# Kernel optimization log

Measured on AMD Instinct MI355X. Metric: run time of the kernel, lower is better.

The kernel has to match this reference:

```python
import jax, jax.numpy as jnp
import numpy as np

N = 50000   # nodes
E = 400000  # edges (before self-loops)
F = 128     # num_features
H = 8       # heads (layer 1)
C = 64      # hidden_channels
B = 64      # graphs in batch
K = 10      # num_classes
NEG_SLOPE = 0.2


def setup_inputs() -> dict:
    key = jax.random.key(0)
    ks = jax.random.split(key, 12)
    g = lambda k, shape, fan: jax.random.normal(k, shape, jnp.float32) / np.sqrt(fan).astype(np.float32)
    return {
        "x": jax.random.normal(ks[0], (N, F), jnp.float32),
        "edge_index": jax.random.randint(ks[1], (2, E), 0, N, jnp.int32),
        "batch": jnp.sort(jax.random.randint(ks[2], (N,), 0, B, jnp.int32)),
        "W1": g(ks[3], (F, H * C), F),
        "att_src1": g(ks[4], (H, C), C),
        "att_dst1": g(ks[5], (H, C), C),
        "b1": jnp.zeros((H * C,), jnp.float32),
        "W2": g(ks[6], (H * C, C), H * C),
        "att_src2": g(ks[7], (1, C), C),
        "att_dst2": g(ks[8], (1, C), C),
        "b2": jnp.zeros((C,), jnp.float32),
        "lin1_w": g(ks[9], (C, C), C),
        "lin1_b": jnp.zeros((C,), jnp.float32),
        "lin2_w": g(ks[10], (C, K), C),
        "lin2_b": jnp.zeros((K,), jnp.float32),
    }


def gat_conv(x, src, dst, W, att_src, att_dst, bias):
    """PyG GATConv (self-loops already appended to src/dst). x:[N,Fin] -> [N,H*C]."""
    heads, out_c = att_src.shape
    h = (x @ W).reshape(N, heads, out_c)                      # [N,H,C]
    a_s = jnp.einsum('nhc,hc->nh', h, att_src)                # [N,H]
    a_d = jnp.einsum('nhc,hc->nh', h, att_dst)
    e = jax.nn.leaky_relu(a_s[src] + a_d[dst], NEG_SLOPE)     # [E',H]
    # segment softmax over incoming edges of each destination node
    m = jax.ops.segment_max(e, dst, num_segments=N)
    e = jnp.exp(e - m[dst])
    denom = jax.ops.segment_sum(e, dst, num_segments=N)
    alpha = e / (denom[dst] + 1e-16)                          # [E',H]
    out = jax.ops.segment_sum(h[src] * alpha[:, :, None], dst, num_segments=N)  # [N,H,C]
    return out.reshape(N, heads * out_c) + bias


def reference(x, edge_index, batch, W1, att_src1, att_dst1, b1,
              W2, att_src2, att_dst2, b2, lin1_w, lin1_b, lin2_w, lin2_b):
    loops = jnp.arange(N, dtype=edge_index.dtype)
    src = jnp.concatenate([edge_index[0], loops])
    dst = jnp.concatenate([edge_index[1], loops])

    h = gat_conv(x, src, dst, W1, att_src1, att_dst1, b1)     # [N, H*C]
    h = jax.nn.elu(h)                                         # dropout inactive (eval)
    h = gat_conv(h, src, dst, W2, att_src2, att_dst2, b2)     # [N, C]
    h = jax.nn.elu(h)

    pooled = jax.ops.segment_sum(h, batch, num_segments=B)    # global_add_pool -> [B, C]
    z = jax.nn.elu(pooled @ lin1_w + lin1_b)
    logits = z @ lin2_w + lin2_b
    return jax.nn.log_softmax(logits, axis=-1)
```

## Files before the change

kernel.cpp:

```cpp
#include <hip/hip_runtime.h>
#include <hip/hip_bf16.h>

#define DEV static __device__ __forceinline__

constexpr int F1 = 128;
constexpr int H1 = 8;
constexpr int C  = 64;
constexpr int B  = 64;
constexpr int K  = 10;
constexpr float NEG = 0.2f;

typedef __attribute__((ext_vector_type(8))) short short8;
typedef __attribute__((ext_vector_type(4))) float floatx4;

DEV float b2f(__hip_bfloat16 x) { return __bfloat162float(x); }
DEV float elu1(float v) { return v > 0.f ? v : (__expf(v) - 1.f); }
DEV unsigned short f2bbits(float f) {
  __hip_bfloat16 b = __float2bfloat16(f);
  return *(unsigned short*)&b;
}
DEV float blo(unsigned u) { return __uint_as_float(u << 16); }
DEV float bhi(unsigned u) { return __uint_as_float(u & 0xffff0000u); }
DEV float bu(unsigned short u) { return __uint_as_float(((unsigned)u) << 16); }
DEV unsigned pack2(float lo, float hi) {
  return (unsigned)f2bbits(lo) | ((unsigned)f2bbits(hi) << 16);
}

DEV int detect_dev(const void* xraw, int* lds) {
  if (threadIdx.x == 0) {
    const __hip_bfloat16* xb = (const __hip_bfloat16*)xraw;
    int bad = 0;
    for (int i = 0; i < 128; ++i) {
      float v = b2f(xb[2 * i]);
      if (!(fabsf(v) < 1e4f)) bad++;
    }
    *lds = (bad < 13) ? 1 : 0;
  }
  __syncthreads();
  return *lds;
}

#define CVT(p, i) (isbf ? b2f(((const __hip_bfloat16*)(p))[i]) : ((const float*)(p))[i])

__global__ void fused_prep_kernel(const void* x_raw, const void* w1raw,
                                  const void* as1r, const void* ad1r, const void* b1r,
                                  const void* w2raw,
                                  const void* as2r, const void* ad2r, const void* b2r,
                                  const void* l1wr, const void* l1br,
                                  const void* l2wr, const void* l2br,
                                  unsigned short* __restrict__ xbf,
                                  unsigned short* __restrict__ w1frag,
                                  unsigned short* __restrict__ w2frag,
                                  float* __restrict__ wts,
                                  int* __restrict__ deg,
                                  float* __restrict__ pooled,
                                  int nX, int N) {
  __shared__ int fl;
  int isbf = detect_dev(x_raw, &fl);
  int gid = blockIdx.x * 256 + threadIdx.x;
  int stride = gridDim.x * 256;

  if (isbf) {
    const unsigned short* src = (const unsigned short*)x_raw;
    for (int i = gid; i < nX; i += stride) xbf[i] = src[i];
  } else {
    const float* src = (const float*)x_raw;
    for (int i = gid; i < nX; i += stride) xbf[i] = f2bbits(src[i]);
  }
  for (int i = gid; i < 512;  i += stride) wts[0    + i] = CVT(as1r, i);
  for (int i = gid; i < 512;  i += stride) wts[512  + i] = CVT(ad1r, i);
  for (int i = gid; i < 512;  i += stride) wts[1024 + i] = CVT(b1r, i);
  for (int i = gid; i < 64;   i += stride) wts[1536 + i] = CVT(as2r, i);
  for (int i = gid; i < 64;   i += stride) wts[1600 + i] = CVT(ad2r, i);
  for (int i = gid; i < 64;   i += stride) wts[1664 + i] = CVT(b2r, i);
  for (int i = gid; i < 4096; i += stride) wts[1728 + i] = CVT(l1wr, i);
  for (int i = gid; i < 64;   i += stride) wts[5824 + i] = CVT(l1br, i);
  for (int i = gid; i < 640;  i += stride) wts[5888 + i] = CVT(l2wr, i);
  for (int i = gid; i < 10;   i += stride) wts[6528 + i] = CVT(l2br, i);
  for (int t = gid; t < 8192; t += stride) {
    int lane = t & 63, ks = (t >> 6) & 3, nt = t >> 8;
    for (int j = 0; j < 8; ++j) {
      int k = ks * 32 + (lane >> 4) * 8 + j;
      int n = nt * 16 + (lane & 15);
      w1frag[t * 8 + j] = f2bbits(CVT(w1raw, k * 512 + n));
    }
  }
  for (int t = gid; t < 4096; t += stride) {
    int lane = t & 63, nt = (t >> 6) & 3, ks = t >> 8;
    for (int j = 0; j < 8; ++j) {
      int k = ks * 32 + (lane >> 4) * 8 + j;
      int n = nt * 16 + (lane & 15);
      w2frag[t * 8 + j] = f2bbits(CVT(w2raw, k * 64 + n));
    }
  }
  for (int i = gid; i < N; i += stride) deg[i] = 0;
  for (int i = gid; i < B * C; i += stride) pooled[i] = 0.f;
}

__global__ void deg_count_kernel(const int* __restrict__ ei, int E, int Etot,
                                 int* __restrict__ deg) {
  int e = blockIdx.x * blockDim.x + threadIdx.x;
  if (e >= Etot) return;
  int d = (e < E) ? ei[E + e] : e - E;
  atomicAdd(&deg[d], 1);
}

__global__ void scan_block_kernel(const int* __restrict__ deg,
                                  int* __restrict__ local,
                                  int* __restrict__ bsum, int N) {
  __shared__ int tmp[256];
  int t = threadIdx.x;
  int i = blockIdx.x * 256 + t;
  int v = (i < N) ? deg[i] : 0;
  tmp[t] = v;
  __syncthreads();
  for (int off = 1; off < 256; off <<= 1) {
    int u = (t >= off) ? tmp[t - off] : 0;
    __syncthreads();
    tmp[t] += u;
    __syncthreads();
  }
  if (i < N) local[i] = tmp[t] - v;
  if (t == 255) bsum[blockIdx.x] = tmp[255];
}

__global__ void scan_sums_kernel(int* __restrict__ bsum, int nb) {
  __shared__ int tmp[256];
  int t = threadIdx.x;
  int v0 = (t < nb) ? bsum[t] : 0;
  tmp[t] = v0;
  __syncthreads();
  for (int off = 1; off < 256; off <<= 1) {
    int u = (t >= off) ? tmp[t - off] : 0;
    __syncthreads();
    tmp[t] += u;
    __syncthreads();
  }
  if (t < nb) bsum[t] = tmp[t] - v0;
}

__global__ void scan_add_kernel(const int* __restrict__ local,
                                const int* __restrict__ bsum,
                                int* __restrict__ rowptr,
                                int* __restrict__ cursor, int N, int Etot) {
  int i = blockIdx.x * 256 + threadIdx.x;
  if (i < N) {
    int r = local[i] + bsum[i >> 8];
    rowptr[i] = r;
    cursor[i] = r;
  }
  if (i == 0) rowptr[N] = Etot;
}

__global__ void csr_fill_kernel(const int* __restrict__ ei, int E, int Etot,
                                int* __restrict__ cursor, int* __restrict__ col) {
  int e = blockIdx.x * blockDim.x + threadIdx.x;
  if (e >= Etot) return;
  int s, d;
  if (e < E) { s = ei[e]; d = ei[E + e]; } else { s = d = e - E; }
  int pos = atomicAdd(&cursor[d], 1);
  col[pos] = s;
}

__global__ __launch_bounds__(256) void gemm1_mfma_kernel(
    const unsigned short* __restrict__ xbf,
    const unsigned short* __restrict__ W1frag,
    const float* __restrict__ att_src,
    const float* __restrict__ att_dst,
    unsigned short* __restrict__ h1,
    float* __restrict__ a_s, float* __restrict__ a_d,
    int N) {
  __shared__ __align__(16) unsigned short Xls[64 * 136];
  int t = threadIdx.x;
  int w = t >> 6, lane = t & 63;
  int quad = lane >> 4, l16 = lane & 15;
  int blkbase = blockIdx.x * 64;
  int rowbase = blkbase + w * 16;

  for (int idx = t; idx < 1024; idx += 256) {
    int row = idx >> 4, c = idx & 15;
    int rg = blkbase + row; if (rg >= N) rg = N - 1;
    *(uint4*)&Xls[row * 136 + c * 8] =
        *(const uint4*)(xbf + (size_t)rg * 128 + c * 8);
  }
  __syncthreads();

  short8 afr[4];
  {
    int rl = w * 16 + l16;
#pragma unroll
    for (int ks = 0; ks < 4; ++ks)
      afr[ks] = *(const short8*)&Xls[rl * 136 + ks * 32 + quad * 8];
  }

  for (int hp = 0; hp < 4; ++hp) {
    floatx4 acc[8] = {};
    const unsigned short* Bp = W1frag + (size_t)hp * 16384;
#pragma unroll
    for (int nt = 0; nt < 8; ++nt)
#pragma unroll
      for (int ks = 0; ks < 4; ++ks) {
        short8 b = *(const short8*)&Bp[((nt * 4 + ks) * 64 + lane) * 8];
        acc[nt] = __builtin_amdgcn_mfma_f32_16x16x32_bf16(afr[ks], b, acc[nt], 0, 0, 0);
      }

    float asw[8], adw[8];
#pragma unroll
    for (int nt = 0; nt < 8; ++nt) {
      asw[nt] = att_src[hp * 128 + nt * 16 + l16];
      adw[nt] = att_dst[hp * 128 + nt * 16 + l16];
    }
    float ps[2][4] = {}, pd[2][4] = {};
#pragma unroll
    for (int nt = 0; nt < 8; ++nt) {
      int hl = nt >> 2;
#pragma unroll
      for (int r = 0; r < 4; ++r) {
        float v = acc[nt][r];
        int row = rowbase + quad * 4 + r;
        if (row < N)
          h1[(size_t)row * 512 + hp * 128 + nt * 16 + l16] = f2bbits(v);
        ps[hl][r] += v * asw[nt];
        pd[hl][r] += v * adw[nt];
      }
    }
#pragma unroll
    for (int hl = 0; hl < 2; ++hl)
#pragma unroll
      for (int r = 0; r < 4; ++r) {
        float p = ps[hl][r], q = pd[hl][r];
#pragma unroll
        for (int off = 1; off < 16; off <<= 1) {
          p += __shfl_xor(p, off);
          q += __shfl_xor(q, off);
        }
        int row = rowbase + quad * 4 + r;
        if (l16 == 0 && row < N) {
          a_s[(size_t)row * 8 + hp * 2 + hl] = p;
          a_d[(size_t)row * 8 + hp * 2 + hl] = q;
        }
      }
  }
}

__global__ __launch_bounds__(256) void gemm2_mfma_kernel(
    const unsigned short* __restrict__ x2bf,
    const unsigned short* __restrict__ W2frag,
    const float* __restrict__ att_src,
    const float* __restrict__ att_dst,
    unsigned short* __restrict__ h2,
    float* __restrict__ a_s, float* __restrict__ a_d,
    int N) {
  int t = threadIdx.x;
  int w = t >> 6, lane = t & 63;
  int quad = lane >> 4, l16 = lane & 15;
  int rowbase = blockIdx.x * 64 + w * 16;

  floatx4 acc[4] = {};
  int r0 = rowbase + l16; if (r0 >= N) r0 = N - 1;
  const unsigned short* p0 = x2bf + (size_t)r0 * 512 + quad * 8;
#pragma unroll
  for (int ks = 0; ks < 16; ++ks) {
    short8 a0 = *(const short8*)(p0 + ks * 32);
#pragma unroll
    for (int nt = 0; nt < 4; ++nt) {
      short8 b = *(const short8*)&W2frag[((ks * 4 + nt) * 64 + lane) * 8];
      acc[nt] = __builtin_amdgcn_mfma_f32_16x16x32_bf16(a0, b, acc[nt], 0, 0, 0);
    }
  }

  float asw[4], adw[4];
#pragma unroll
  for (int nt = 0; nt < 4; ++nt) {
    asw[nt] = att_src[nt * 16 + l16];
    adw[nt] = att_dst[nt * 16 + l16];
  }
  float ps[4] = {}, pd[4] = {};
#pragma unroll
  for (int nt = 0; nt < 4; ++nt)
#pragma unroll
    for (int r = 0; r < 4; ++r) {
      float v = acc[nt][r];
      int row = rowbase + quad * 4 + r;
      if (row < N) h2[(size_t)row * 64 + nt * 16 + l16] = f2bbits(v);
      ps[r] += v * asw[nt];
      pd[r] += v * adw[nt];
    }
#pragma unroll
  for (int r = 0; r < 4; ++r) {
    float p = ps[r], q = pd[r];
#pragma unroll
    for (int off = 1; off < 16; off <<= 1) {
      p += __shfl_xor(p, off);
      q += __shfl_xor(q, off);
    }
    int row = rowbase + quad * 4 + r;
    if (l16 == 0 && row < N) {
      a_s[row] = p;
      a_d[row] = q;
    }
  }
}

__global__ void gat_agg8_kernel(const int* __restrict__ rowptr,
                                const int* __restrict__ col,
                                const float* __restrict__ a_s,
                                const float* __restrict__ a_d,
                                const unsigned short* __restrict__ hfeat,
                                const float* __restrict__ bias,
                                unsigned short* __restrict__ out, int N) {
  int wave = threadIdx.x >> 6, lane = threadIdx.x & 63;
  int d = blockIdx.x * 4 + wave;
  if (d >= N) return;
  int beg = rowptr[d], end = rowptr[d + 1];
  int hh = lane >> 3;
  float adh = a_d[(size_t)d * 8 + hh];

  const uint4* hf = (const uint4*)hfeat;
  float acc[8] = {};
  float wsum = 0.f;
#pragma unroll 4
  for (int i = beg; i < end; ++i) {
    int s = col[i];
    float e = a_s[(size_t)s * 8 + hh] + adh;
    e = e > 0.f ? e : NEG * e;
    float wv = __expf(e);
    wsum += wv;
    uint4 q = hf[(size_t)s * 64 + lane];
    acc[0] += wv * blo(q.x); acc[1] += wv * bhi(q.x);
    acc[2] += wv * blo(q.y); acc[3] += wv * bhi(q.y);
    acc[4] += wv * blo(q.z); acc[5] += wv * bhi(q.z);
    acc[6] += wv * blo(q.w); acc[7] += wv * bhi(q.w);
  }
  float winv = 1.f / (wsum + 1e-16f);
  const float4* b4 = (const float4*)bias;
  float4 b0 = b4[2 * lane], b1 = b4[2 * lane + 1];
  float v0 = elu1(acc[0] * winv + b0.x), v1 = elu1(acc[1] * winv + b0.y);
  float v2 = elu1(acc[2] * winv + b0.z), v3 = elu1(acc[3] * winv + b0.w);
  float v4 = elu1(acc[4] * winv + b1.x), v5 = elu1(acc[5] * winv + b1.y);
  float v6 = elu1(acc[6] * winv + b1.z), v7 = elu1(acc[7] * winv + b1.w);
  uint4 o;
  o.x = pack2(v0, v1); o.y = pack2(v2, v3);
  o.z = pack2(v4, v5); o.w = pack2(v6, v7);
  ((uint4*)out)[(size_t)d * 64 + lane] = o;
}

__global__ void gat_agg1_kernel(const int* __restrict__ rowptr,
                                const int* __restrict__ col,
                                const float* __restrict__ a_s,
                                const float* __restrict__ a_d,
                                const unsigned short* __restrict__ hfeat,
                                const float* __restrict__ bias,
                                unsigned short* __restrict__ out, int N) {
  int wave = threadIdx.x >> 6, lane = threadIdx.x & 63;
  int d = blockIdx.x * 4 + wave;
  if (d >= N) return;
  int beg = rowptr[d], end = rowptr[d + 1];
  int half = lane >> 5, l32 = lane & 31;
  float adv = a_d[d];
  const unsigned* hfu = (const unsigned*)hfeat;
  float acc0 = 0.f, acc1 = 0.f, wsum = 0.f;
#pragma unroll 2
  for (int i = beg + half; i < end; i += 2) {
    int s = col[i];
    float v = a_s[s] + adv;
    v = v > 0.f ? v : NEG * v;
    float wv = __expf(v);
    wsum += wv;
    unsigned u = hfu[(size_t)s * 32 + l32];
    acc0 += wv * blo(u);
    acc1 += wv * bhi(u);
  }
  acc0 += __shfl_xor(acc0, 32);
  acc1 += __shfl_xor(acc1, 32);
  wsum += __shfl_xor(wsum, 32);
  float winv = 1.f / (wsum + 1e-16f);
  float r0 = elu1(acc0 * winv + bias[2 * l32]);
  float r1 = elu1(acc1 * winv + bias[2 * l32 + 1]);
  if (half == 0)
    ((unsigned*)out)[(size_t)d * 32 + l32] = pack2(r0, r1);
}

__global__ void pool_kernel(const unsigned short* __restrict__ out2,
                            const int* __restrict__ batch,
                            float* __restrict__ pooled, int N) {
  int wave = threadIdx.x >> 6, lane = threadIdx.x & 63;
  int seg = blockIdx.x * 4 + wave;
  int start = seg * 16;
  if (start >= N) return;
  int end = min(start + 16, N);
  int cur = batch[start];
  float acc = 0.f;
  for (int n = start; n < end; ++n) {
    int bn = batch[n];
    if (bn != cur) {
      unsafeAtomicAdd(&pooled[cur * 64 + lane], acc);
      acc = 0.f; cur = bn;
    }
    acc += bu(out2[(size_t)n * 64 + lane]);
  }
  unsafeAtomicAdd(&pooled[cur * 64 + lane], acc);
}

__global__ void head_kernel(const float* __restrict__ pooled,
                            const float* __restrict__ lin1_w,
                            const float* __restrict__ lin1_b,
                            const float* __restrict__ lin2_w,
                            const float* __restrict__ lin2_b,
                            const void* __restrict__ x_raw,
                            void* __restrict__ outv) {
  __shared__ float P[B * C];
  __shared__ float Z[B * C];
  __shared__ float L[B * K];
  __shared__ int fl;
  int isbf = detect_dev(x_raw, &fl);
  int t = threadIdx.x;
  for (int i = t; i < B * C; i += 512) P[i] = pooled[i];
  __syncthreads();
  for (int i = t; i < B * C; i += 512) {
    int r = i >> 6, c = i & 63;
    float acc = lin1_b[c];
    for (int k = 0; k < C; ++k) acc += P[r * C + k] * lin1_w[k * C + c];
    Z[i] = elu1(acc);
  }
  __syncthreads();
  for (int i = t; i < B * K; i += 512) {
    int r = i / K, c = i - r * K;
    float acc = lin2_b[c];
    for (int k = 0; k < C; ++k) acc += Z[r * C + k] * lin2_w[k * K + c];
    L[i] = acc;
  }
  __syncthreads();
  if (t < B) {
    float mx = -1e30f;
    for (int c = 0; c < K; ++c) mx = fmaxf(mx, L[t * K + c]);
    float s = 0.f;
    for (int c = 0; c < K; ++c) s += __expf(L[t * K + c] - mx);
    float lse = mx + __logf(s);
    for (int c = 0; c < K; ++c) {
      float val = L[t * K + c] - lse;
      if (isbf) ((__hip_bfloat16*)outv)[t * K + c] = __float2bfloat16(val);
      else      ((float*)outv)[t * K + c] = val;
    }
  }
}

extern "C" void kernel_launch(void* const* d_in, const int* in_sizes, int n_in,
                              void* d_out, int out_size, void* d_ws, size_t ws_size,
                              hipStream_t stream) {
  const void* x_raw = d_in[0];
  const int*  ei    = (const int*)d_in[1];
  const int*  batch = (const int*)d_in[2];

  const int N    = in_sizes[2];
  const int E    = in_sizes[1] / 2;
  const int Etot = E + N;
  const int nb   = (N + 255) / 256;

  float* ws   = (float*)d_ws;
  size_t off  = 0;

  float* wts = ws + off; off += 6544;
  float* as1w = wts + 0;
  float* ad1w = wts + 512;
  float* b1w  = wts + 1024;
  float* as2w = wts + 1536;
  float* ad2w = wts + 1600;
  float* b2w  = wts + 1664;
  float* l1w  = wts + 1728;
  float* l1b  = wts + 5824;
  float* l2w  = wts + 5888;
  float* l2b  = wts + 6528;

  unsigned short* xbf    = (unsigned short*)(ws + off); off += (size_t)N * 64;
  unsigned short* w1frag = (unsigned short*)(ws + off); off += 32768;
  unsigned short* w2frag = (unsigned short*)(ws + off); off += 16384;
  unsigned short* h1bf   = (unsigned short*)(ws + off); off += (size_t)N * 256;
  unsigned short* out1bf = (unsigned short*)(ws + off); off += (size_t)N * 256;
  unsigned short* h2bf   = (unsigned short*)(ws + off); off += (size_t)N * 32;
  unsigned short* out2bf = (unsigned short*)(ws + off); off += (size_t)N * 32;
  float* as1  = ws + off; off += (size_t)N * H1;
  float* ad1  = ws + off; off += (size_t)N * H1;
  float* as2  = ws + off; off += (size_t)N;
  float* ad2  = ws + off; off += (size_t)N;
  float* pooled = ws + off; off += (size_t)B * C;

  int* ibase  = (int*)(ws + off);
  int* deg    = ibase;                 ibase += N;
  int* cursor = ibase;                 ibase += N;
  int* rowptr = ibase;                 ibase += N + 1;
  int* locals = ibase;                 ibase += N;
  int* bsum   = ibase;                 ibase += 256;
  int* col    = ibase;                 ibase += Etot;

  fused_prep_kernel<<<1024, 256, 0, stream>>>(
      x_raw, d_in[3], d_in[4], d_in[5], d_in[6], d_in[7], d_in[8], d_in[9],
      d_in[10], d_in[11], d_in[12], d_in[13], d_in[14],
      xbf, w1frag, w2frag, wts, deg, pooled, in_sizes[0], N);

  deg_count_kernel<<<(Etot + 255) / 256, 256, 0, stream>>>(ei, E, Etot, deg);
  scan_block_kernel<<<nb, 256, 0, stream>>>(deg, locals, bsum, N);
  scan_sums_kernel<<<1, 256, 0, stream>>>(bsum, nb);
  scan_add_kernel<<<nb, 256, 0, stream>>>(locals, bsum, rowptr, cursor, N, Etot);
  csr_fill_kernel<<<(Etot + 255) / 256, 256, 0, stream>>>(ei, E, Etot, cursor, col);

  gemm1_mfma_kernel<<<(N + 63) / 64, 256, 0, stream>>>(xbf, w1frag, as1w, ad1w,
                                                       h1bf, as1, ad1, N);
  gat_agg8_kernel<<<(N + 3) / 4, 256, 0, stream>>>(rowptr, col, as1, ad1, h1bf, b1w, out1bf, N);

  gemm2_mfma_kernel<<<(N + 63) / 64, 256, 0, stream>>>(out1bf, w2frag, as2w, ad2w,
                                                       h2bf, as2, ad2, N);
  gat_agg1_kernel<<<(N + 3) / 4, 256, 0, stream>>>(rowptr, col, as2, ad2, h2bf, b2w, out2bf, N);

  pool_kernel<<<(N + 63) / 64, 256, 0, stream>>>(out2bf, batch, pooled, N);
  head_kernel<<<1, 512, 0, stream>>>(pooled, l1w, l1b, l2w, l2b, x_raw, (void*)d_out);
}
```

Before: 332.3 us.

## Fuse degree count into GEMM1, merge scan kernels, widen agg1, parallelize head

Degree counting now runs as extra blocks appended to the GEMM1 launch, so the atomic histogram overlaps the MFMA work and one launch disappears. The scan-of-block-sums and scan-add kernels are merged: each block redundantly rescans the block sums and applies its own offset. The layer-2 aggregation splits each edge list across four lane groups with 8-byte loads instead of two with 4-byte loads. The head kernel moves from one 512-thread block to one 64-thread block per graph. Together these cut launch count and serial work, at the cost of redundant scans per block.

```diff
diff --git a/kernel.cpp b/kernel.cpp
--- a/kernel.cpp
+++ b/kernel.cpp
@@ -97,81 +97,27 @@
   for (int i = gid; i < B * C; i += stride) pooled[i] = 0.f;
 }
 
-__global__ void deg_count_kernel(const int* __restrict__ ei, int E, int Etot,
-                                 int* __restrict__ deg) {
-  int e = blockIdx.x * blockDim.x + threadIdx.x;
-  if (e >= Etot) return;
-  int d = (e < E) ? ei[E + e] : e - E;
-  atomicAdd(&deg[d], 1);
-}
-
-__global__ void scan_block_kernel(const int* __restrict__ deg,
-                                  int* __restrict__ local,
-                                  int* __restrict__ bsum, int N) {
-  __shared__ int tmp[256];
-  int t = threadIdx.x;
-  int i = blockIdx.x * 256 + t;
-  int v = (i < N) ? deg[i] : 0;
-  tmp[t] = v;
-  __syncthreads();
-  for (int off = 1; off < 256; off <<= 1) {
-    int u = (t >= off) ? tmp[t - off] : 0;
-    __syncthreads();
-    tmp[t] += u;
-    __syncthreads();
-  }
-  if (i < N) local[i] = tmp[t] - v;
-  if (t == 255) bsum[blockIdx.x] = tmp[255];
-}
-
-__global__ void scan_sums_kernel(int* __restrict__ bsum, int nb) {
-  __shared__ int tmp[256];
-  int t = threadIdx.x;
-  int v0 = (t < nb) ? bsum[t] : 0;
-  tmp[t] = v0;
-  __syncthreads();
-  for (int off = 1; off < 256; off <<= 1) {
-    int u = (t >= off) ? tmp[t - off] : 0;
-    __syncthreads();
-    tmp[t] += u;
-    __syncthreads();
-  }
-  if (t < nb) bsum[t] = tmp[t] - v0;
-}
-
-__global__ void scan_add_kernel(const int* __restrict__ local,
-                                const int* __restrict__ bsum,
-                                int* __restrict__ rowptr,
-                                int* __restrict__ cursor, int N, int Etot) {
-  int i = blockIdx.x * 256 + threadIdx.x;
-  if (i < N) {
-    int r = local[i] + bsum[i >> 8];
-    rowptr[i] = r;
-    cursor[i] = r;
-  }
-  if (i == 0) rowptr[N] = Etot;
-}
-
-__global__ void csr_fill_kernel(const int* __restrict__ ei, int E, int Etot,
-                                int* __restrict__ cursor, int* __restrict__ col) {
-  int e = blockIdx.x * blockDim.x + threadIdx.x;
-  if (e >= Etot) return;
-  int s, d;
-  if (e < E) { s = ei[e]; d = ei[E + e]; } else { s = d = e - E; }
-  int pos = atomicAdd(&cursor[d], 1);
-  col[pos] = s;
-}
-
-__global__ __launch_bounds__(256) void gemm1_mfma_kernel(
+__global__ __launch_bounds__(256) void gemm1_deg_kernel(
     const unsigned short* __restrict__ xbf,
     const unsigned short* __restrict__ W1frag,
     const float* __restrict__ att_src,
     const float* __restrict__ att_dst,
     unsigned short* __restrict__ h1,
     float* __restrict__ a_s, float* __restrict__ a_d,
-    int N) {
+    const int* __restrict__ ei, int E, int Etot,
+    int* __restrict__ deg, int gb, int N) {
   __shared__ __align__(16) unsigned short Xls[64 * 136];
   int t = threadIdx.x;
+
+  if ((int)blockIdx.x >= gb) {
+    int e = ((int)blockIdx.x - gb) * 256 + t;
+    if (e < Etot) {
+      int d = (e < E) ? ei[E + e] : e - E;
+      atomicAdd(&deg[d], 1);
+    }
+    return;
+  }
+
   int w = t >> 6, lane = t & 63;
   int quad = lane >> 4, l16 = lane & 15;
   int blkbase = blockIdx.x * 64;
@@ -241,6 +187,62 @@
         }
       }
   }
+}
+
+__global__ void scan_block_kernel(const int* __restrict__ deg,
+                                  int* __restrict__ local,
+                                  int* __restrict__ bsum, int N) {
+  __shared__ int tmp[256];
+  int t = threadIdx.x;
+  int i = blockIdx.x * 256 + t;
+  int v = (i < N) ? deg[i] : 0;
+  tmp[t] = v;
+  __syncthreads();
+  for (int off = 1; off < 256; off <<= 1) {
+    int u = (t >= off) ? tmp[t - off] : 0;
+    __syncthreads();
+    tmp[t] += u;
+    __syncthreads();
+  }
+  if (i < N) local[i] = tmp[t] - v;
+  if (t == 255) bsum[blockIdx.x] = tmp[255];
+}
+
+__global__ void scan_finish_kernel(const int* __restrict__ local,
+                                   const int* __restrict__ bsum, int nb,
+                                   int* __restrict__ rowptr,
+                                   int* __restrict__ cursor, int N, int Etot) {
+  __shared__ int tmp[256];
+  __shared__ int offs;
+  int t = threadIdx.x;
+  int v0 = (t < nb) ? bsum[t] : 0;
+  tmp[t] = v0;
+  __syncthreads();
+  for (int off = 1; off < 256; off <<= 1) {
+    int u = (t >= off) ? tmp[t - off] : 0;
+    __syncthreads();
+    tmp[t] += u;
+    __syncthreads();
+  }
+  if (t == (int)blockIdx.x) offs = tmp[t] - v0;
+  __syncthreads();
+  int i = blockIdx.x * 256 + t;
+  if (i < N) {
+    int r = local[i] + offs;
+    rowptr[i] = r;
+    cursor[i] = r;
+  }
+  if (i == 0) rowptr[N] = Etot;
+}
+
+__global__ void csr_fill_kernel(const int* __restrict__ ei, int E, int Etot,
+                                int* __restrict__ cursor, int* __restrict__ col) {
+  int e = blockIdx.x * blockDim.x + threadIdx.x;
+  if (e >= Etot) return;
+  int s, d;
+  if (e < E) { s = ei[e]; d = ei[E + e]; } else { s = d = e - E; }
+  int pos = atomicAdd(&cursor[d], 1);
+  col[pos] = s;
 }
 
 __global__ __launch_bounds__(256) void gemm2_mfma_kernel(
@@ -356,29 +358,36 @@
   int d = blockIdx.x * 4 + wave;
   if (d >= N) return;
   int beg = rowptr[d], end = rowptr[d + 1];
-  int half = lane >> 5, l32 = lane & 31;
+  int qg = lane >> 4, l16 = lane & 15;
   float adv = a_d[d];
-  const unsigned* hfu = (const unsigned*)hfeat;
-  float acc0 = 0.f, acc1 = 0.f, wsum = 0.f;
+  const uint2* hfu = (const uint2*)hfeat;
+  float acc[4] = {};
+  float wsum = 0.f;
 #pragma unroll 2
-  for (int i = beg + half; i < end; i += 2) {
+  for (int i = beg + qg; i < end; i += 4) {
     int s = col[i];
     float v = a_s[s] + adv;
     v = v > 0.f ? v : NEG * v;
     float wv = __expf(v);
     wsum += wv;
-    unsigned u = hfu[(size_t)s * 32 + l32];
-    acc0 += wv * blo(u);
-    acc1 += wv * bhi(u);
-  }
-  acc0 += __shfl_xor(acc0, 32);
-  acc1 += __shfl_xor(acc1, 32);
-  wsum += __shfl_xor(wsum, 32);
+    uint2 u = hfu[(size_t)s * 16 + l16];
+    acc[0] += wv * blo(u.x); acc[1] += wv * bhi(u.x);
+    acc[2] += wv * blo(u.y); acc[3] += wv * bhi(u.y);
+  }
+#pragma unroll
+  for (int off = 16; off <= 32; off <<= 1) {
+#pragma unroll
+    for (int j = 0; j < 4; ++j) acc[j] += __shfl_xor(acc[j], off);
+    wsum += __shfl_xor(wsum, off);
+  }
   float winv = 1.f / (wsum + 1e-16f);
-  float r0 = elu1(acc0 * winv + bias[2 * l32]);
-  float r1 = elu1(acc1 * winv + bias[2 * l32 + 1]);
-  if (half == 0)
-    ((unsigned*)out)[(size_t)d * 32 + l32] = pack2(r0, r1);
+  float4 bb = ((const float4*)bias)[l16];
+  float r0 = elu1(acc[0] * winv + bb.x), r1 = elu1(acc[1] * winv + bb.y);
+  float r2 = elu1(acc[2] * winv + bb.z), r3 = elu1(acc[3] * winv + bb.w);
+  if (qg == 0) {
+    uint2 o; o.x = pack2(r0, r1); o.y = pack2(r2, r3);
+    ((uint2*)out)[(size_t)d * 16 + l16] = o;
+  }
 }
 
 __global__ void pool_kernel(const unsigned short* __restrict__ out2,
@@ -409,39 +418,37 @@
                             const float* __restrict__ lin2_b,
                             const void* __restrict__ x_raw,
                             void* __restrict__ outv) {
-  __shared__ float P[B * C];
-  __shared__ float Z[B * C];
-  __shared__ float L[B * K];
+  __shared__ float P[C];
+  __shared__ float Zs[C];
+  __shared__ float Ls[K];
+  __shared__ float lse_s;
   __shared__ int fl;
   int isbf = detect_dev(x_raw, &fl);
-  int t = threadIdx.x;
-  for (int i = t; i < B * C; i += 512) P[i] = pooled[i];
-  __syncthreads();
-  for (int i = t; i < B * C; i += 512) {
-    int r = i >> 6, c = i & 63;
-    float acc = lin1_b[c];
-    for (int k = 0; k < C; ++k) acc += P[r * C + k] * lin1_w[k * C + c];
-    Z[i] = elu1(acc);
-  }
-  __syncthreads();
-  for (int i = t; i < B * K; i += 512) {
-    int r = i / K, c = i - r * K;
-    float acc = lin2_b[c];
-    for (int k = 0; k < C; ++k) acc += Z[r * C + k] * lin2_w[k * K + c];
-    L[i] = acc;
-  }
-  __syncthreads();
-  if (t < B) {
+  int g = blockIdx.x, t = threadIdx.x;
+  P[t] = pooled[g * C + t];
+  __syncthreads();
+  float acc = lin1_b[t];
+  for (int k = 0; k < C; ++k) acc += P[k] * lin1_w[k * C + t];
+  Zs[t] = elu1(acc);
+  __syncthreads();
+  if (t < K) {
+    float a = lin2_b[t];
+    for (int k = 0; k < C; ++k) a += Zs[k] * lin2_w[k * K + t];
+    Ls[t] = a;
+  }
+  __syncthreads();
+  if (t == 0) {
     float mx = -1e30f;
-    for (int c = 0; c < K; ++c) mx = fmaxf(mx, L[t * K + c]);
+    for (int c = 0; c < K; ++c) mx = fmaxf(mx, Ls[c]);
     float s = 0.f;
-    for (int c = 0; c < K; ++c) s += __expf(L[t * K + c] - mx);
-    float lse = mx + __logf(s);
-    for (int c = 0; c < K; ++c) {
-      float val = L[t * K + c] - lse;
-      if (isbf) ((__hip_bfloat16*)outv)[t * K + c] = __float2bfloat16(val);
-      else      ((float*)outv)[t * K + c] = val;
-    }
+    for (int c = 0; c < K; ++c) s += __expf(Ls[c] - mx);
+    lse_s = mx + __logf(s);
+  }
+  __syncthreads();
+  if (t < K) {
+    float val = Ls[t] - lse_s;
+    if (isbf) ((__hip_bfloat16*)outv)[g * K + t] = __float2bfloat16(val);
+    else      ((float*)outv)[g * K + t] = val;
   }
 }
 
@@ -498,14 +505,18 @@
       d_in[10], d_in[11], d_in[12], d_in[13], d_in[14],
       xbf, w1frag, w2frag, wts, deg, pooled, in_sizes[0], N);
 
-  deg_count_kernel<<<(Etot + 255) / 256, 256, 0, stream>>>(ei, E, Etot, deg);
+  {
+    int gb = (N + 63) / 64;
+    int db = (Etot + 255) / 256;
+    gemm1_deg_kernel<<<gb + db, 256, 0, stream>>>(xbf, w1frag, as1w, ad1w,
+                                                  h1bf, as1, ad1,
+                                                  ei, E, Etot, deg, gb, N);
+  }
+
   scan_block_kernel<<<nb, 256, 0, stream>>>(deg, locals, bsum, N);
-  scan_sums_kernel<<<1, 256, 0, stream>>>(bsum, nb);
-  scan_add_kernel<<<nb, 256, 0, stream>>>(locals, bsum, rowptr, cursor, N, Etot);
+  scan_finish_kernel<<<nb, 256, 0, stream>>>(locals, bsum, nb, rowptr, cursor, N, Etot);
   csr_fill_kernel<<<(Etot + 255) / 256, 256, 0, stream>>>(ei, E, Etot, cursor, col);
 
-  gemm1_mfma_kernel<<<(N + 63) / 64, 256, 0, stream>>>(xbf, w1frag, as1w, ad1w,
-                                                       h1bf, as1, ad1, N);
   gat_agg8_kernel<<<(N + 3) / 4, 256, 0, stream>>>(rowptr, col, as1, ad1, h1bf, b1w, out1bf, N);
 
   gemm2_mfma_kernel<<<(N + 63) / 64, 256, 0, stream>>>(out1bf, w2frag, as2w, ad2w,
@@ -513,5 +524,5 @@
   gat_agg1_kernel<<<(N + 3) / 4, 256, 0, stream>>>(rowptr, col, as2, ad2, h2bf, b2w, out2bf, N);
 
   pool_kernel<<<(N + 63) / 64, 256, 0, stream>>>(out2bf, batch, pooled, N);
-  head_kernel<<<1, 512, 0, stream>>>(pooled, l1w, l1b, l2w, l2b, x_raw, (void*)d_out);
-}
+  head_kernel<<<B, 64, 0, stream>>>(pooled, l1w, l1b, l2w, l2b, x_raw, (void*)d_out);
+}
```

New measurement: 314.1 us. 5.5% less time.
